# Performance work log

Hardware: AMD Instinct MI355X
Metric: run time of the kernel (lower is better)

The kernel has to match this reference:

```python
import jax, jax.numpy as jnp
import numpy as np
from jax import lax


def _conv2d(x, w, b, stride):
    # x: [B,C,H,W], w: [O,I,kh,kw], b: [O]
    y = lax.conv_general_dilated(
        x, w, window_strides=(stride, stride), padding='VALID',
        dimension_numbers=('NCHW', 'OIHW', 'NCHW'))
    return y + b[None, :, None, None]


def setup_inputs() -> dict:
    key = jax.random.key(0)
    ks = jax.random.split(key, 4)
    B, C, H, W = 8, 128, 128, 128
    x = jax.random.normal(ks[0], (B, C, H, W), dtype=jnp.float32)
    # conv weights, scaled like torch default init (~1/sqrt(fan_in))
    Wq = jax.random.normal(ks[1], (C, C, 2, 2), dtype=jnp.float32) / np.sqrt(C * 4)
    Wk = jax.random.normal(ks[2], (C, C, 2, 2), dtype=jnp.float32) / np.sqrt(C * 4)
    Wv = jax.random.normal(ks[3], (C, C, 1, 1), dtype=jnp.float32) / np.sqrt(C)
    bq = jnp.zeros((C,), dtype=jnp.float32)
    bk = jnp.zeros((C,), dtype=jnp.float32)
    bv = jnp.zeros((C,), dtype=jnp.float32)
    return {'x': x, 'Wq': Wq, 'bq': bq, 'Wk': Wk, 'bk': bk, 'Wv': Wv, 'bv': bv}


def reference(x, Wq, bq, Wk, bk, Wv, bv):
    B, C, H, W = x.shape
    # query/key: 2x2 stride-2 convs -> [B, C, (H//2)*(W//2)]
    q = _conv2d(x, Wq, bq, 2).reshape(B, C, -1)
    k = _conv2d(x, Wk, bk, 2).reshape(B, C, -1)
    # value: 1x1 conv -> [B, C, H*W]
    v = _conv2d(x, Wv, bv, 1).reshape(B, C, -1)
    # energy: [B, C, C]
    energy = jnp.einsum('bcn,bdn->bcd', q, k)
    # max-subtract trick: softmax over (row_max - energy)
    energy_new = jnp.max(energy, axis=-1, keepdims=True) - energy
    attention = jax.nn.softmax(energy_new, axis=-1)
    out = jnp.einsum('bcd,bdn->bcn', attention, v)
    return out.reshape(B, C, H, W)
```

## Files before the change

kernel.cpp:

```cpp
#include <hip/hip_runtime.h>
#include <math.h>


typedef float f32x4 __attribute__((ext_vector_type(4)));
typedef short s16x8 __attribute__((ext_vector_type(8)));

__device__ __forceinline__ unsigned short f2bf(float f) {
  union { float f; unsigned u; } v; v.f = f;
  unsigned r = v.u + 0x7FFFu + ((v.u >> 16) & 1u);
  return (unsigned short)(r >> 16);
}
__device__ __forceinline__ float bf2f(unsigned short h) {
  union { unsigned u; float f; } v; v.u = ((unsigned)h) << 16;
  return v.f;
}
__device__ __forceinline__ unsigned pack2(unsigned short a, unsigned short b) {
  return (unsigned)a | ((unsigned)b << 16);
}

__global__ __launch_bounds__(256) void k_prep(
    const float* __restrict__ Wq, const float* __restrict__ Wk,
    unsigned short* __restrict__ Wth, unsigned short* __restrict__ Wtl) {
  const int f = (blockIdx.x * 256 + threadIdx.x) * 4;
  const int row = f >> 9;
  const int k   = f & 511;
  const float* src = (row < 128) ? &Wq[row * 512 + k] : &Wk[(row - 128) * 512 + k];
  float4 v = *(const float4*)src;
  unsigned short h0 = f2bf(v.x), h1 = f2bf(v.y), h2 = f2bf(v.z), h3 = f2bf(v.w);
  unsigned short l0 = f2bf(v.x - bf2f(h0)), l1 = f2bf(v.y - bf2f(h1));
  unsigned short l2 = f2bf(v.z - bf2f(h2)), l3 = f2bf(v.w - bf2f(h3));
  const int di = (k >> 5) * 8192 + row * 32 + (k & 31);
  *(ushort4*)&Wth[di] = make_ushort4(h0, h1, h2, h3);
  *(ushort4*)&Wtl[di] = make_ushort4(l0, l1, l2, l3);
}

__global__ __launch_bounds__(256, 2) void k_conv_energy(
    const float* __restrict__ x,
    const unsigned short* __restrict__ Wth, const unsigned short* __restrict__ Wtl,
    const float* __restrict__ bq, const float* __restrict__ bk,
    float* __restrict__ epart) {
  __shared__ unsigned short LDS[32768];
  unsigned short* Th = LDS;
  unsigned short* Tl = LDS + 16384;

  const int t = threadIdx.x;
  const int nt = blockIdx.x, b = blockIdx.y;
  const int w = t >> 6, lane = t & 63;
  const int lrow = lane & 15, lkb = lane >> 4;

  const int pp = t >> 4;
  const int ci_l = pp >> 1, kh = pp & 1;
  const int i16 = t & 15;
  const int klb = ci_l * 4 + kh * 2;
  const float* xb = x + ((size_t)b << 21);
  const float* xrow = xb + (size_t)ci_l * 16384 + (2 * nt + kh) * 128 + 2 * i16;

  f32x4 acc[4][4];
#pragma unroll
  for (int m = 0; m < 4; ++m)
#pragma unroll
    for (int n = 0; n < 4; ++n) acc[m][n] = (f32x4){0.f, 0.f, 0.f, 0.f};

  s16x8 pfh[2][4], pfl[2][4];
  const int aoff = (w * 64 + lrow) * 32 + lkb * 8;

#pragma unroll
  for (int m = 0; m < 4; ++m) {
    pfh[0][m] = *(const s16x8*)&Wth[aoff + m * 512];
    pfl[0][m] = *(const s16x8*)&Wtl[aoff + m * 512];
  }
  {
#pragma unroll
    for (int g = 0; g < 4; ++g) {
      const int n = i16 + 16 * g;
      float2 v = *(const float2*)&xrow[32 * g];
      unsigned short hx = f2bf(v.x), hy = f2bf(v.y);
      *(unsigned*)&LDS[n * 40 + klb]        = pack2(hx, hy);
      *(unsigned*)&LDS[2560 + n * 40 + klb] = pack2(f2bf(v.x - bf2f(hx)),
                                                    f2bf(v.y - bf2f(hy)));
    }
  }
  __syncthreads();

#pragma unroll
  for (int step = 0; step < 16; ++step) {
    const int cb = step & 1;
    if (step < 15) {
      const unsigned short* Wh_n = Wth + (step + 1) * 8192;
      const unsigned short* Wl_n = Wtl + (step + 1) * 8192;
#pragma unroll
      for (int m = 0; m < 4; ++m) {
        pfh[cb ^ 1][m] = *(const s16x8*)&Wh_n[aoff + m * 512];
        pfl[cb ^ 1][m] = *(const s16x8*)&Wl_n[aoff + m * 512];
      }
    }
    float2 pv0, pv1, pv2, pv3;
    if (step < 15) {
      const float* xr = xrow + (size_t)(step + 1) * 8 * 16384;
      pv0 = *(const float2*)&xr[0];
      pv1 = *(const float2*)&xr[32];
      pv2 = *(const float2*)&xr[64];
      pv3 = *(const float2*)&xr[96];
    }
    const unsigned short* Bh = LDS + cb * 5120;
    const unsigned short* Bl = Bh + 2560;
    s16x8 bfh[4], bfl[4];
#pragma unroll
    for (int nf = 0; nf < 4; ++nf) {
      const int bidx = (nf * 16 + lrow) * 40 + lkb * 8;
      bfh[nf] = *(const s16x8*)&Bh[bidx];
      bfl[nf] = *(const s16x8*)&Bl[bidx];
    }
#pragma unroll
    for (int m = 0; m < 4; ++m)
#pragma unroll
      for (int n = 0; n < 4; ++n) {
        acc[m][n] = __builtin_amdgcn_mfma_f32_16x16x32_bf16(pfh[cb][m], bfh[n], acc[m][n], 0, 0, 0);
        acc[m][n] = __builtin_amdgcn_mfma_f32_16x16x32_bf16(pfh[cb][m], bfl[n], acc[m][n], 0, 0, 0);
        acc[m][n] = __builtin_amdgcn_mfma_f32_16x16x32_bf16(pfl[cb][m], bfh[n], acc[m][n], 0, 0, 0);
      }
    if (step < 15) {
      unsigned short* Nh = LDS + (cb ^ 1) * 5120;
      unsigned short* Nl = Nh + 2560;
      {
        const int n = i16;
        unsigned short hx = f2bf(pv0.x), hy = f2bf(pv0.y);
        *(unsigned*)&Nh[n * 40 + klb] = pack2(hx, hy);
        *(unsigned*)&Nl[n * 40 + klb] = pack2(f2bf(pv0.x - bf2f(hx)), f2bf(pv0.y - bf2f(hy)));
      }
      {
        const int n = i16 + 16;
        unsigned short hx = f2bf(pv1.x), hy = f2bf(pv1.y);
        *(unsigned*)&Nh[n * 40 + klb] = pack2(hx, hy);
        *(unsigned*)&Nl[n * 40 + klb] = pack2(f2bf(pv1.x - bf2f(hx)), f2bf(pv1.y - bf2f(hy)));
      }
      {
        const int n = i16 + 32;
        unsigned short hx = f2bf(pv2.x), hy = f2bf(pv2.y);
        *(unsigned*)&Nh[n * 40 + klb] = pack2(hx, hy);
        *(unsigned*)&Nl[n * 40 + klb] = pack2(f2bf(pv2.x - bf2f(hx)), f2bf(pv2.y - bf2f(hy)));
      }
      {
        const int n = i16 + 48;
        unsigned short hx = f2bf(pv3.x), hy = f2bf(pv3.y);
        *(unsigned*)&Nh[n * 40 + klb] = pack2(hx, hy);
        *(unsigned*)&Nl[n * 40 + klb] = pack2(f2bf(pv3.x - bf2f(hx)), f2bf(pv3.y - bf2f(hy)));
      }
    }
    __syncthreads();
  }

  const float* biasp = (w < 2) ? bq : bk;
  const int rb = (w & 1) * 64;
  float biasr[16];
#pragma unroll
  for (int m = 0; m < 4; ++m)
#pragma unroll
    for (int i = 0; i < 4; ++i)
      biasr[m * 4 + i] = biasp[rb + m * 16 + (lane >> 4) * 4 + i];

#pragma unroll
  for (int m = 0; m < 4; ++m) {
    const int r0 = w * 64 + m * 16 + (lane >> 4) * 4;
#pragma unroll
    for (int n = 0; n < 4; ++n) {
      const int c = n * 16 + lrow;
      const int c8 = c >> 3, c7 = c & 7;
#pragma unroll
      for (int i = 0; i < 4; ++i) {
        const int r = r0 + i;
        const float vv = acc[m][n][i] + biasr[m * 4 + i];
        const unsigned short h = f2bf(vv);
        const unsigned short l = f2bf(vv - bf2f(h));
        const int ad = r * 64 + (((c8 ^ (r & 7))) << 3) + c7;
        Th[ad] = h;
        Tl[ad] = l;
      }
    }
  }
  __syncthreads();

  f32x4 e[4][4];
#pragma unroll
  for (int m = 0; m < 4; ++m)
#pragma unroll
    for (int n = 0; n < 4; ++n) e[m][n] = (f32x4){0.f, 0.f, 0.f, 0.f};

  const int mrow0 = (w >> 1) * 64;
  const int nrow0 = 128 + (w & 1) * 64;
#pragma unroll
  for (int ks = 0; ks < 2; ++ks) {
    const int c8 = ks * 4 + lkb;
    s16x8 qh[4], ql[4], kh8[4], kl8[4];
#pragma unroll
    for (int m = 0; m < 4; ++m) {
      const int r = mrow0 + m * 16 + lrow;
      const int ad = r * 64 + ((c8 ^ (r & 7)) << 3);
      qh[m] = *(const s16x8*)&Th[ad];
      ql[m] = *(const s16x8*)&Tl[ad];
    }
#pragma unroll
    for (int n = 0; n < 4; ++n) {
      const int r = nrow0 + n * 16 + lrow;
      const int ad = r * 64 + ((c8 ^ (r & 7)) << 3);
      kh8[n] = *(const s16x8*)&Th[ad];
      kl8[n] = *(const s16x8*)&Tl[ad];
    }
#pragma unroll
    for (int m = 0; m < 4; ++m)
#pragma unroll
      for (int n = 0; n < 4; ++n) {
        e[m][n] = __builtin_amdgcn_mfma_f32_16x16x32_bf16(qh[m], kh8[n], e[m][n], 0, 0, 0);
        e[m][n] = __builtin_amdgcn_mfma_f32_16x16x32_bf16(qh[m], kl8[n], e[m][n], 0, 0, 0);
        e[m][n] = __builtin_amdgcn_mfma_f32_16x16x32_bf16(ql[m], kh8[n], e[m][n], 0, 0, 0);
      }
  }
  float* ep = epart + ((size_t)b * 64 + nt) * 16384;
#pragma unroll
  for (int m = 0; m < 4; ++m) {
    const int qr = (w >> 1) * 64 + m * 16 + (lane >> 4) * 4;
#pragma unroll
    for (int n = 0; n < 4; ++n) {
      const int kr = (w & 1) * 64 + n * 16 + lrow;
#pragma unroll
      for (int i = 0; i < 4; ++i) ep[(size_t)(qr + i) * 128 + kr] = e[m][n][i];
    }
  }
}

__global__ __launch_bounds__(256) void k_softmax_M(
    const float* __restrict__ epart, const float* __restrict__ Wv,
    const float* __restrict__ bv, float* __restrict__ Mbuf,
    float* __restrict__ outbb) {
  __shared__ float As[4][128];
  const int t = threadIdx.x;
  const int wid = t >> 6, lane = t & 63;
  const int b = blockIdx.x >> 5;
  const int c = (blockIdx.x & 31) * 4 + wid;
  const int d0 = lane * 2;

  float2 s = make_float2(0.f, 0.f);
#pragma unroll 4
  for (int p = 0; p < 64; ++p) {
    float2 e = *(const float2*)&epart[((size_t)b * 64 + p) * 16384 + c * 128 + d0];
    s.x += e.x; s.y += e.y;
  }
  float mn = fminf(s.x, s.y);
#pragma unroll
  for (int off = 1; off < 64; off <<= 1) mn = fminf(mn, __shfl_xor(mn, off));
  const float p0 = expf(mn - s.x);
  const float p1 = expf(mn - s.y);
  float tot = p0 + p1;
#pragma unroll
  for (int off = 1; off < 64; off <<= 1) tot += __shfl_xor(tot, off);
  const float inv = 1.f / tot;
  const float a0 = p0 * inv, a1 = p1 * inv;

  const float2 bvv = *(const float2*)&bv[d0];
  float ob = a0 * bvv.x + a1 * bvv.y;
#pragma unroll
  for (int off = 1; off < 64; off <<= 1) ob += __shfl_xor(ob, off);
  if (lane == 0) outbb[b * 128 + c] = ob;

  As[wid][d0] = a0;
  As[wid][d0 + 1] = a1;
  float m0 = 0.f, m1 = 0.f;
#pragma unroll 4
  for (int d = 0; d < 128; ++d) {
    const float a = As[wid][d];
    const float2 wv = *(const float2*)&Wv[d * 128 + d0];
    m0 = fmaf(a, wv.x, m0);
    m1 = fmaf(a, wv.y, m1);
  }
  *(float2*)&Mbuf[(size_t)b * 16384 + c * 128 + d0] = make_float2(m0, m1);
}

__global__ __launch_bounds__(256) void k_out(
    const float* __restrict__ x, const float* __restrict__ Mbuf,
    const float* __restrict__ outbb, float* __restrict__ out) {
  __shared__ unsigned short Ms[128 * 40];
  __shared__ unsigned short Xs[128 * 40];
  const int t = threadIdx.x;
  const int nt = blockIdx.x, b = blockIdx.y;
  const int wid = t >> 6, lane = t & 63;
  const int wr = wid >> 1, wc = wid & 1;
  const int lrow = lane & 15, lkb = lane >> 4;
  const int am = t >> 1, ak0 = (t & 1) * 16;
  const int xkl = (t >> 5) * 4;
  const int xc0 = (t & 31) * 4;

  const float* xb = x + ((size_t)b << 21);
  const float* Mb = Mbuf + (size_t)b * 16384;
  float* ob = out + ((size_t)b << 21);

  f32x4 acc[4][4];
#pragma unroll
  for (int m = 0; m < 4; ++m)
#pragma unroll
    for (int n = 0; n < 4; ++n) acc[m][n] = (f32x4){0.f, 0.f, 0.f, 0.f};

  for (int step = 0; step < 4; ++step) {
    const int kk = step * 32;
    {
      float w[16];
      *(float4*)&w[0]  = *(const float4*)&Mb[am * 128 + kk + ak0];
      *(float4*)&w[4]  = *(const float4*)&Mb[am * 128 + kk + ak0 + 4];
      *(float4*)&w[8]  = *(const float4*)&Mb[am * 128 + kk + ak0 + 8];
      *(float4*)&w[12] = *(const float4*)&Mb[am * 128 + kk + ak0 + 12];
      unsigned short hs[16];
#pragma unroll
      for (int i = 0; i < 16; ++i) hs[i] = f2bf(w[i]);
      *(uint4*)&Ms[am * 40 + ak0]     = *(uint4*)&hs[0];
      *(uint4*)&Ms[am * 40 + ak0 + 8] = *(uint4*)&hs[8];
    }
#pragma unroll
    for (int q = 0; q < 4; ++q) {
      const int kl = xkl + q;
      float4 v = *(const float4*)&xb[(size_t)(kk + kl) * 16384 + nt * 128 + xc0];
      Xs[(xc0 + 0) * 40 + kl] = f2bf(v.x);
      Xs[(xc0 + 1) * 40 + kl] = f2bf(v.y);
      Xs[(xc0 + 2) * 40 + kl] = f2bf(v.z);
      Xs[(xc0 + 3) * 40 + kl] = f2bf(v.w);
    }
    __syncthreads();
    s16x8 af[4], bf[4];
#pragma unroll
    for (int m = 0; m < 4; ++m)
      af[m] = *(const s16x8*)&Ms[(wr * 64 + m * 16 + lrow) * 40 + lkb * 8];
#pragma unroll
    for (int n = 0; n < 4; ++n)
      bf[n] = *(const s16x8*)&Xs[(wc * 64 + n * 16 + lrow) * 40 + lkb * 8];
#pragma unroll
    for (int m = 0; m < 4; ++m)
#pragma unroll
      for (int n = 0; n < 4; ++n)
        acc[m][n] = __builtin_amdgcn_mfma_f32_16x16x32_bf16(af[m], bf[n], acc[m][n], 0, 0, 0);
    __syncthreads();
  }
#pragma unroll
  for (int m = 0; m < 4; ++m) {
    const int r0 = wr * 64 + m * 16 + (lane >> 4) * 4;
#pragma unroll
    for (int n = 0; n < 4; ++n) {
      const int gc = nt * 128 + wc * 64 + n * 16 + (lane & 15);
#pragma unroll
      for (int i = 0; i < 4; ++i) {
        const int row = r0 + i;
        ob[(size_t)row * 16384 + gc] = acc[m][n][i] + outbb[b * 128 + row];
      }
    }
  }
}

extern "C" void kernel_launch(void* const* d_in, const int* in_sizes, int n_in,
                              void* d_out, int out_size, void* d_ws, size_t ws_size,
                              hipStream_t stream) {
  const float* x  = (const float*)d_in[0];
  const float* Wq = (const float*)d_in[1];
  const float* bq = (const float*)d_in[2];
  const float* Wk = (const float*)d_in[3];
  const float* bk = (const float*)d_in[4];
  const float* Wv = (const float*)d_in[5];
  const float* bv = (const float*)d_in[6];
  float* out = (float*)d_out;
  char* ws = (char*)d_ws;

  float* epart = (float*)ws;
  float* Mbuf  = (float*)(ws + 33554432);
  float* outbb = (float*)(ws + 34078720);
  unsigned short* Wth = (unsigned short*)(ws + 34082816);
  unsigned short* Wtl = (unsigned short*)(ws + 34344960);

  hipLaunchKernelGGL(k_prep, dim3(128), dim3(256), 0, stream, Wq, Wk, Wth, Wtl);
  hipLaunchKernelGGL(k_conv_energy, dim3(64, 8), dim3(256), 0, stream,
                     x, Wth, Wtl, bq, bk, epart);
  hipLaunchKernelGGL(k_softmax_M, dim3(256), dim3(256), 0, stream,
                     epart, Wv, bv, Mbuf, outbb);
  hipLaunchKernelGGL(k_out, dim3(128, 8), dim3(256), 0, stream,
                     x, Mbuf, outbb, out);
}
```

Measured before the change: 87.01 us.

## Deepen software pipeline in QK conv GEMM to prefetch two steps ahead

Restructures the main K-loop of the query/key conv GEMM so global loads of x and the weight fragments are issued two steps ahead, while LDS B-fragments for the next step are read into registers before the MFMAs of the current step. The LDS write of converted data now happens at the top of each step, ahead of the barrier, so global-load latency has a whole step of MFMA work to hide behind. This costs more registers for the extra double-buffered fragments and float2 staging, which may lower occupancy.

```diff
diff --git a/kernel.cpp b/kernel.cpp
--- a/kernel.cpp
+++ b/kernel.cpp
@@ -62,93 +62,92 @@
     for (int n = 0; n < 4; ++n) acc[m][n] = (f32x4){0.f, 0.f, 0.f, 0.f};
 
   s16x8 pfh[2][4], pfl[2][4];
+  s16x8 bfh[2][4], bfl[2][4];
+  float2 pv[2][4];
   const int aoff = (w * 64 + lrow) * 32 + lkb * 8;
 
 #pragma unroll
   for (int m = 0; m < 4; ++m) {
     pfh[0][m] = *(const s16x8*)&Wth[aoff + m * 512];
     pfl[0][m] = *(const s16x8*)&Wtl[aoff + m * 512];
-  }
+    pfh[1][m] = *(const s16x8*)&Wth[8192 + aoff + m * 512];
+    pfl[1][m] = *(const s16x8*)&Wtl[8192 + aoff + m * 512];
+  }
+#pragma unroll
+  for (int g = 0; g < 4; ++g) pv[1][g] = *(const float2*)&xrow[32 * g];
   {
+    unsigned short* Nh = LDS;
+    unsigned short* Nl = LDS + 2560;
 #pragma unroll
     for (int g = 0; g < 4; ++g) {
       const int n = i16 + 16 * g;
-      float2 v = *(const float2*)&xrow[32 * g];
-      unsigned short hx = f2bf(v.x), hy = f2bf(v.y);
-      *(unsigned*)&LDS[n * 40 + klb]        = pack2(hx, hy);
-      *(unsigned*)&LDS[2560 + n * 40 + klb] = pack2(f2bf(v.x - bf2f(hx)),
-                                                    f2bf(v.y - bf2f(hy)));
-    }
-  }
+      unsigned short hx = f2bf(pv[1][g].x), hy = f2bf(pv[1][g].y);
+      *(unsigned*)&Nh[n * 40 + klb] = pack2(hx, hy);
+      *(unsigned*)&Nl[n * 40 + klb] = pack2(f2bf(pv[1][g].x - bf2f(hx)),
+                                            f2bf(pv[1][g].y - bf2f(hy)));
+    }
+  }
+#pragma unroll
+  for (int g = 0; g < 4; ++g)
+    pv[1][g] = *(const float2*)&xrow[(size_t)8 * 16384 + 32 * g];
   __syncthreads();
+#pragma unroll
+  for (int nf = 0; nf < 4; ++nf) {
+    const int bidx = (nf * 16 + lrow) * 40 + lkb * 8;
+    bfh[0][nf] = *(const s16x8*)&LDS[bidx];
+    bfl[0][nf] = *(const s16x8*)&LDS[2560 + bidx];
+  }
 
 #pragma unroll
   for (int step = 0; step < 16; ++step) {
-    const int cb = step & 1;
+    const int cur = step & 1;
     if (step < 15) {
-      const unsigned short* Wh_n = Wth + (step + 1) * 8192;
-      const unsigned short* Wl_n = Wtl + (step + 1) * 8192;
+      unsigned short* Nh = LDS + (cur ^ 1) * 5120;
+      unsigned short* Nl = Nh + 2560;
+#pragma unroll
+      for (int g = 0; g < 4; ++g) {
+        const int n = i16 + 16 * g;
+        unsigned short hx = f2bf(pv[cur ^ 1][g].x), hy = f2bf(pv[cur ^ 1][g].y);
+        *(unsigned*)&Nh[n * 40 + klb] = pack2(hx, hy);
+        *(unsigned*)&Nl[n * 40 + klb] = pack2(f2bf(pv[cur ^ 1][g].x - bf2f(hx)),
+                                              f2bf(pv[cur ^ 1][g].y - bf2f(hy)));
+      }
+    }
+    __syncthreads();
+    if (step < 15) {
+      const unsigned short* Bh = LDS + (cur ^ 1) * 5120;
+      const unsigned short* Bl = Bh + 2560;
+#pragma unroll
+      for (int nf = 0; nf < 4; ++nf) {
+        const int bidx = (nf * 16 + lrow) * 40 + lkb * 8;
+        bfh[cur ^ 1][nf] = *(const s16x8*)&Bh[bidx];
+        bfl[cur ^ 1][nf] = *(const s16x8*)&Bl[bidx];
+      }
+    }
+    if (step < 14) {
+#pragma unroll
+      for (int g = 0; g < 4; ++g)
+        pv[cur][g] = *(const float2*)&xrow[(size_t)(step + 2) * 8 * 16384 + 32 * g];
+    }
+#pragma unroll
+    for (int m = 0; m < 4; ++m)
+#pragma unroll
+      for (int n = 0; n < 4; ++n) {
+        acc[m][n] = __builtin_amdgcn_mfma_f32_16x16x32_bf16(pfh[cur][m], bfh[cur][n], acc[m][n], 0, 0, 0);
+        acc[m][n] = __builtin_amdgcn_mfma_f32_16x16x32_bf16(pfh[cur][m], bfl[cur][n], acc[m][n], 0, 0, 0);
+        acc[m][n] = __builtin_amdgcn_mfma_f32_16x16x32_bf16(pfl[cur][m], bfh[cur][n], acc[m][n], 0, 0, 0);
+      }
+    if (step < 14) {
+      const unsigned short* Wh_n = Wth + (step + 2) * 8192;
+      const unsigned short* Wl_n = Wtl + (step + 2) * 8192;
 #pragma unroll
       for (int m = 0; m < 4; ++m) {
-        pfh[cb ^ 1][m] = *(const s16x8*)&Wh_n[aoff + m * 512];
-        pfl[cb ^ 1][m] = *(const s16x8*)&Wl_n[aoff + m * 512];
-      }
-    }
-    float2 pv0, pv1, pv2, pv3;
-    if (step < 15) {
-      const float* xr = xrow + (size_t)(step + 1) * 8 * 16384;
-      pv0 = *(const float2*)&xr[0];
-      pv1 = *(const float2*)&xr[32];
-      pv2 = *(const float2*)&xr[64];
-      pv3 = *(const float2*)&xr[96];
-    }
-    const unsigned short* Bh = LDS + cb * 5120;
-    const unsigned short* Bl = Bh + 2560;
-    s16x8 bfh[4], bfl[4];
-#pragma unroll
-    for (int nf = 0; nf < 4; ++nf) {
-      const int bidx = (nf * 16 + lrow) * 40 + lkb * 8;
-      bfh[nf] = *(const s16x8*)&Bh[bidx];
-      bfl[nf] = *(const s16x8*)&Bl[bidx];
-    }
-#pragma unroll
-    for (int m = 0; m < 4; ++m)
-#pragma unroll
-      for (int n = 0; n < 4; ++n) {
-        acc[m][n] = __builtin_amdgcn_mfma_f32_16x16x32_bf16(pfh[cb][m], bfh[n], acc[m][n], 0, 0, 0);
-        acc[m][n] = __builtin_amdgcn_mfma_f32_16x16x32_bf16(pfh[cb][m], bfl[n], acc[m][n], 0, 0, 0);
-        acc[m][n] = __builtin_amdgcn_mfma_f32_16x16x32_bf16(pfl[cb][m], bfh[n], acc[m][n], 0, 0, 0);
-      }
-    if (step < 15) {
-      unsigned short* Nh = LDS + (cb ^ 1) * 5120;
-      unsigned short* Nl = Nh + 2560;
-      {
-        const int n = i16;
-        unsigned short hx = f2bf(pv0.x), hy = f2bf(pv0.y);
-        *(unsigned*)&Nh[n * 40 + klb] = pack2(hx, hy);
-        *(unsigned*)&Nl[n * 40 + klb] = pack2(f2bf(pv0.x - bf2f(hx)), f2bf(pv0.y - bf2f(hy)));
-      }
-      {
-        const int n = i16 + 16;
-        unsigned short hx = f2bf(pv1.x), hy = f2bf(pv1.y);
-        *(unsigned*)&Nh[n * 40 + klb] = pack2(hx, hy);
-        *(unsigned*)&Nl[n * 40 + klb] = pack2(f2bf(pv1.x - bf2f(hx)), f2bf(pv1.y - bf2f(hy)));
-      }
-      {
-        const int n = i16 + 32;
-        unsigned short hx = f2bf(pv2.x), hy = f2bf(pv2.y);
-        *(unsigned*)&Nh[n * 40 + klb] = pack2(hx, hy);
-        *(unsigned*)&Nl[n * 40 + klb] = pack2(f2bf(pv2.x - bf2f(hx)), f2bf(pv2.y - bf2f(hy)));
-      }
-      {
-        const int n = i16 + 48;
-        unsigned short hx = f2bf(pv3.x), hy = f2bf(pv3.y);
-        *(unsigned*)&Nh[n * 40 + klb] = pack2(hx, hy);
-        *(unsigned*)&Nl[n * 40 + klb] = pack2(f2bf(pv3.x - bf2f(hx)), f2bf(pv3.y - bf2f(hy)));
-      }
-    }
-    __syncthreads();
-  }
+        pfh[cur][m] = *(const s16x8*)&Wh_n[aoff + m * 512];
+        pfl[cur][m] = *(const s16x8*)&Wl_n[aoff + m * 512];
+      }
+    }
+  }
+  __syncthreads();
 
   const float* biasp = (w < 2) ? bq : bk;
   const int rb = (w & 1) * 64;
```

Result: no change. 87.04 us (+0.0%).
